# Kernel optimization log

Measured on AMD Instinct MI355X. Metric: run time of the kernel, lower is better.

Reference implementation:

```python
import jax, jax.numpy as jnp
import numpy as np

N = 4096        # nodes
F_IN = 256      # in_features
F_OUT = 64      # out_features
H = 64          # lstm_out_features
MAX_DEG = 64    # max neighbor count == max packed seq length
ALPHA = 0.2     # leaky relu negative slope
NEG = -9e15


def setup_inputs() -> dict:
    key = jax.random.key(0)
    ks = jax.random.split(key, 8)
    h = jax.random.normal(ks[0], (N, F_IN), dtype=jnp.float32)
    # per-node neighbor counts in [1, MAX_DEG]
    seq_length = jax.random.randint(ks[1], (N,), 1, MAX_DEG + 1, dtype=jnp.int32)
    # adjacency with exactly seq_length[i] ones in row i
    r = jax.random.uniform(ks[2], (N, N))
    ranks = jnp.argsort(jnp.argsort(-r, axis=1), axis=1)
    adj = (ranks < seq_length[:, None]).astype(jnp.float32)
    # parameters (xavier-ish scale)
    W = jax.random.normal(ks[3], (F_IN, F_OUT), dtype=jnp.float32) * (2.0 / (F_IN + F_OUT)) ** 0.5
    a = jax.random.normal(ks[4], (2 * F_OUT, 1), dtype=jnp.float32) * 0.1
    # backward-direction LSTM weights (torch gate order i,f,g,o); forward dir is unused in output
    w_ih = jax.random.normal(ks[5], (4 * H, F_OUT), dtype=jnp.float32) * 0.1
    w_hh = jax.random.normal(ks[6], (4 * H, H), dtype=jnp.float32) * 0.1
    b_ih = jnp.zeros((4 * H,), dtype=jnp.float32)
    b_hh = jnp.zeros((4 * H,), dtype=jnp.float32)
    return {"h": h, "adj": adj, "seq_length": seq_length, "W": W, "a": a,
            "w_ih": w_ih, "w_hh": w_hh, "b_ih": b_ih, "b_hh": b_hh}


def reference(h, adj, seq_length, W, a, w_ih, w_hh, b_ih, b_hh):
    n = h.shape[0]
    Wh = h @ W                                   # [N, F_OUT]
    # e[i,j] = leakyrelu(a_left . Wh_i + a_right . Wh_j)  (same math as O(N^2) concat)
    a1, a2 = a[:F_OUT, 0], a[F_OUT:, 0]
    e = jax.nn.leaky_relu((Wh @ a1)[:, None] + (Wh @ a2)[None, :], negative_slope=ALPHA)
    att = jax.nn.softmax(jnp.where(adj > 0, e, NEG), axis=1)   # [N, N]
    Wh2 = att @ Wh                               # aggregated node features [N, F_OUT]
    # sort neighbors by descending attention; LSTM only reads the first seq_length[i] <= MAX_DEG
    order = jnp.argsort(-att, axis=1)[:, :MAX_DEG]            # [N, T]
    seq = Wh2[order]                              # [N, T, F_OUT]
    # backward LSTM direction == run forward over the length-reversed sequence
    t = jnp.arange(MAX_DEG)
    rev_idx = jnp.clip(seq_length[:, None] - 1 - t[None, :], 0)
    rev = jnp.take_along_axis(seq, rev_idx[:, :, None], axis=1)  # [N, T, F_OUT]
    mask = t[None, :] < seq_length[:, None]                       # [N, T]

    def cell(carry, xm):
        hs, cs = carry
        x, m = xm                                 # x: [N, F_OUT], m: [N]
        gates = x @ w_ih.T + hs @ w_hh.T + b_ih + b_hh
        i, f, g, o = jnp.split(gates, 4, axis=1)
        c_new = jax.nn.sigmoid(f) * cs + jax.nn.sigmoid(i) * jnp.tanh(g)
        h_new = jax.nn.sigmoid(o) * jnp.tanh(c_new)
        m = m[:, None]
        return (jnp.where(m, h_new, hs), jnp.where(m, c_new, cs)), None

    init = (jnp.zeros((n, H), Wh.dtype), jnp.zeros((n, H), Wh.dtype))
    xs = (jnp.swapaxes(rev, 0, 1), mask.T)        # time-major
    (hn, _), _ = jax.lax.scan(cell, init, xs)
    return hn                                     # [N, H]  == torch hn[-1] (backward dir)
```

## Files before the change

kernel.cpp:

```cpp
#include <hip/hip_runtime.h>
#include <hip/hip_bf16.h>
#include <math.h>

#define N_NODES 4096
#define F_INN   256
#define F_OUTT  64
#define HID     64
#define MAXDEG  64

typedef __attribute__((ext_vector_type(8))) short bf16x8;
typedef __attribute__((ext_vector_type(4))) float f32x4;

__device__ int    g_mode;
__device__ int    g_anyArr[64];
__device__ float  g_Wh [N_NODES * F_OUTT];
__device__ float  g_s1 [N_NODES];
__device__ float  g_s2 [N_NODES];
__device__ int    g_rev[N_NODES * MAXDEG];
__device__ int    g_perm[N_NODES];
__device__ int    g_nbr[N_NODES * MAXDEG];
__device__ int    g_cnt[N_NODES];
__device__ float4 g_GX [N_NODES * F_OUTT];

__device__ __forceinline__ float bf2f(unsigned short u) {
  union { unsigned int i; float f; } v; v.i = ((unsigned int)u) << 16; return v.f;
}
__device__ __forceinline__ unsigned short f2bf(float f) {
  union { __hip_bfloat16 b; unsigned short u; } v; v.b = __float2bfloat16(f); return v.u;
}

__device__ __forceinline__ float bcastf(float v, int l) {
  return __int_as_float(__builtin_amdgcn_readlane(__float_as_int(v), l));
}

__device__ __forceinline__ float rcp_fast(float x) { return __builtin_amdgcn_rcpf(x); }

__device__ __forceinline__ float sigm(float x) {
  return rcp_fast(1.f + __expf(-x));
}
__device__ __forceinline__ float tanh_fast(float x) {
  return fmaf(-2.f, rcp_fast(1.f + __expf(2.f * x)), 1.f);
}

__device__ __forceinline__ int mbcnt64(unsigned long long m) {
  return __builtin_amdgcn_mbcnt_hi((unsigned)(m >> 32),
         __builtin_amdgcn_mbcnt_lo((unsigned)(m & 0xFFFFFFFFull), 0));
}

__device__ __forceinline__ bf16x8 zfrag() {
  bf16x8 z;
  #pragma unroll
  for (int i = 0; i < 8; i++) z[i] = 0;
  return z;
}

__device__ __forceinline__ void block_sync_lds() {
  __asm__ volatile("s_waitcnt lgkmcnt(0)" ::: "memory");
  __builtin_amdgcn_s_barrier();
}

#define MFMA16(a, b, c) __builtin_amdgcn_mfma_f32_16x16x32_bf16((a), (b), (c), 0, 0, 0)

__global__ __launch_bounds__(256) void k_detect(const unsigned int* __restrict__ aw) {
  __shared__ int any;
  if (threadIdx.x == 0) any = 0;
  __syncthreads();
  const uint4 v = ((const uint4*)aw)[blockIdx.x * 256 + threadIdx.x];
  int loc = (int)((v.x & 0xFFFFu) | (v.y & 0xFFFFu) | (v.z & 0xFFFFu) | (v.w & 0xFFFFu));
  if (loc) atomicOr(&any, 1);
  __syncthreads();
  if (threadIdx.x == 0) g_anyArr[blockIdx.x] = any;
}

__global__ __launch_bounds__(256) void k_sort(const int* __restrict__ seq) {
  __shared__ int hist[MAXDEG + 1];
  __shared__ int offs[MAXDEG + 1];
  const int tid = threadIdx.x;
  if (tid <= MAXDEG) hist[tid] = 0;
  __syncthreads();
  if (tid == 0) {
    int any = 0;
    for (int b = 0; b < 64; b++) any |= g_anyArr[b];
    g_mode = any ? 1 : 0;
  }
  for (int i = tid; i < N_NODES; i += 256)
    atomicAdd(&hist[min(max(seq[i], 0), MAXDEG)], 1);
  __syncthreads();
  if (tid == 0) {
    int run = 0;
    for (int L = MAXDEG; L >= 0; L--) { offs[L] = run; run += hist[L]; }
  }
  __syncthreads();
  for (int i = tid; i < N_NODES; i += 256) {
    int p = atomicAdd(&offs[min(max(seq[i], 0), MAXDEG)], 1);
    g_perm[p] = i;
  }
}

__global__ __launch_bounds__(256) void k_scan(const void* __restrict__ adj) {
  const bool bf16 = (g_mode == 1);
  const int i = blockIdx.x;
  const int w = threadIdx.x >> 6, lane = threadIdx.x & 63;
  __shared__ int seg[4][MAXDEG];
  __shared__ int scnt[4];

  int base = 0;
  if (bf16) {
    const uint4* ar = (const uint4*)((const unsigned short*)adj + (size_t)i * N_NODES);
    #pragma unroll
    for (int it = 0; it < 2; it++) {
      const uint4 v = ar[w * 128 + it * 64 + lane];
      unsigned word[4] = {v.x, v.y, v.z, v.w};
      bool nz[8];
      #pragma unroll
      for (int k = 0; k < 4; k++) {
        nz[2 * k]     = (word[k] & 0x0000FFFFu) != 0u;
        nz[2 * k + 1] = (word[k] & 0xFFFF0000u) != 0u;
      }
      int pre = 0, tot = 0;
      #pragma unroll
      for (int k = 0; k < 8; k++) {
        unsigned long long bl = __ballot(nz[k]);
        pre += mbcnt64(bl);
        tot += __popcll(bl);
      }
      int loc = 0;
      #pragma unroll
      for (int k = 0; k < 8; k++) {
        if (nz[k]) {
          int p = base + pre + loc;
          if (p < MAXDEG) seg[w][p] = w * 1024 + it * 512 + lane * 8 + k;
          loc++;
        }
      }
      base += tot;
    }
  } else {
    const float4* ar = (const float4*)((const float*)adj + (size_t)i * N_NODES);
    #pragma unroll
    for (int it = 0; it < 4; it++) {
      const float4 v = ar[w * 256 + it * 64 + lane];
      bool nz[4] = {v.x != 0.0f, v.y != 0.0f, v.z != 0.0f, v.w != 0.0f};
      int pre = 0, tot = 0;
      #pragma unroll
      for (int k = 0; k < 4; k++) {
        unsigned long long bl = __ballot(nz[k]);
        pre += mbcnt64(bl);
        tot += __popcll(bl);
      }
      int loc = 0;
      #pragma unroll
      for (int k = 0; k < 4; k++) {
        if (nz[k]) {
          int p = base + pre + loc;
          if (p < MAXDEG) seg[w][p] = w * 1024 + it * 256 + lane * 4 + k;
          loc++;
        }
      }
      base += tot;
    }
  }
  if (lane == 0) scnt[w] = base;
  __syncthreads();
  int off = 0;
  #pragma unroll
  for (int u = 0; u < 4; u++) off += (u < w) ? scnt[u] : 0;
  const int cw = min(scnt[w], MAXDEG);
  if (lane < cw) {
    const int p = off + lane;
    if (p < MAXDEG) g_nbr[i * MAXDEG + p] = seg[w][lane];
  }
  if (threadIdx.x == 0)
    g_cnt[i] = min(scnt[0] + scnt[1] + scnt[2] + scnt[3], MAXDEG);
}

__global__ __launch_bounds__(256) void k_wh(
    const void* __restrict__ h, const void* __restrict__ W, const void* __restrict__ a)
{
  const bool bf16 = (g_mode == 1);
  __shared__ float Ws[F_INN * F_OUTT];
  const int tid = threadIdx.x;
  if (bf16) {
    const ushort4* Wu = (const ushort4*)W;
    for (int v = tid; v < F_INN * F_OUTT / 4; v += 256) {
      ushort4 u = Wu[v];
      ((float4*)Ws)[v] = make_float4(bf2f(u.x), bf2f(u.y), bf2f(u.z), bf2f(u.w));
    }
  } else {
    const float4* Wf = (const float4*)W;
    for (int v = tid; v < F_INN * F_OUTT / 4; v += 256) ((float4*)Ws)[v] = Wf[v];
  }
  __syncthreads();
  const int wave = tid >> 6, lane = tid & 63;
  const int row = blockIdx.x * 4 + wave;
  float hr0, hr1, hr2, hr3;
  if (bf16) {
    ushort4 v = ((const ushort4*)((const unsigned short*)h + row * F_INN))[lane];
    hr0 = bf2f(v.x); hr1 = bf2f(v.y); hr2 = bf2f(v.z); hr3 = bf2f(v.w);
  } else {
    float4 v = ((const float4*)((const float*)h + row * F_INN))[lane];
    hr0 = v.x; hr1 = v.y; hr2 = v.z; hr3 = v.w;
  }
  double acc = 0.0;
  #pragma unroll 8
  for (int l = 0; l < 64; l++) {
    float h0 = bcastf(hr0, l), h1 = bcastf(hr1, l);
    float h2 = bcastf(hr2, l), h3 = bcastf(hr3, l);
    acc += (double)h0 * (double)Ws[(l * 4 + 0) * F_OUTT + lane];
    acc += (double)h1 * (double)Ws[(l * 4 + 1) * F_OUTT + lane];
    acc += (double)h2 * (double)Ws[(l * 4 + 2) * F_OUTT + lane];
    acc += (double)h3 * (double)Ws[(l * 4 + 3) * F_OUTT + lane];
  }
  const float whv = (float)acc;
  g_Wh[row * F_OUTT + lane] = whv;
  float a1, a2;
  if (bf16) {
    a1 = bf2f(((const unsigned short*)a)[lane]);
    a2 = bf2f(((const unsigned short*)a)[F_OUTT + lane]);
  } else {
    a1 = ((const float*)a)[lane];
    a2 = ((const float*)a)[F_OUTT + lane];
  }
  double t1 = (double)whv * (double)a1;
  double t2 = (double)whv * (double)a2;
  #pragma unroll
  for (int off = 32; off > 0; off >>= 1) {
    t1 += __shfl_down(t1, off);
    t2 += __shfl_down(t2, off);
  }
  if (lane == 0) { g_s1[row] = (float)t1; g_s2[row] = (float)t2; }
}

__global__ __launch_bounds__(256) void k_att2(
    const void* __restrict__ w_ih,
    const void* __restrict__ b_ih, const void* __restrict__ b_hh)
{
  const bool bf16 = (g_mode == 1);
  const int wv = threadIdx.x >> 6, lane = threadIdx.x & 63;
  const int i = blockIdx.x * 4 + wv;

  __shared__ int   s_nbr[4][MAXDEG];
  __shared__ float s_att[4][MAXDEG];
  __shared__ int   s_srt[4][MAXDEG];
  __shared__ float s_wh2[4][F_OUTT];
  int*   nbr  = s_nbr[wv];
  float* attp = s_att[wv];
  int*   srt  = s_srt[wv];
  float* wh2  = s_wh2[wv];

  const int L = min(g_cnt[i], MAXDEG);
  int jn = 0;
  if (lane < L) jn = g_nbr[i * MAXDEG + lane] & (N_NODES - 1);
  nbr[lane] = jn;

  const float s2v = g_s2[jn];
  float av;
  {
    float s = g_s1[i] + s2v;
    float e = (s > 0.0f) ? s : 0.2f * s;
    if (lane >= L) e = -3.0e38f;
    float m = e;
    #pragma unroll
    for (int off = 32; off > 0; off >>= 1) m = fmaxf(m, __shfl_xor(m, off));
    float p = (lane < L) ? __expf(e - m) : 0.0f;
    float ssum = p;
    #pragma unroll
    for (int off = 32; off > 0; off >>= 1) ssum += __shfl_xor(ssum, off);
    av = p * rcp_fast(ssum);
    attp[lane] = av;
    int rank = 0;
    for (int qq = 0; qq < L; qq++) {
      float aq = __shfl(av, qq);
      int   jq = __shfl(jn, qq);
      rank += (aq > av || (aq == av && jq < jn)) ? 1 : 0;
    }
    if (lane < L) srt[rank] = jn;
  }
  g_rev[i * MAXDEG + lane] = (lane < L) ? srt[L - 1 - lane] : 0;

  float a0 = 0.f, a1 = 0.f, a2 = 0.f, a3 = 0.f;
  int q = 0;
  for (; q + 4 <= L; q += 4) {
    const int j0 = nbr[q], j1 = nbr[q + 1], j2 = nbr[q + 2], j3 = nbr[q + 3];
    const float t0 = attp[q], t1 = attp[q + 1], t2 = attp[q + 2], t3 = attp[q + 3];
    a0 = fmaf(t0, g_Wh[(size_t)j0 * F_OUTT + lane], a0);
    a1 = fmaf(t1, g_Wh[(size_t)j1 * F_OUTT + lane], a1);
    a2 = fmaf(t2, g_Wh[(size_t)j2 * F_OUTT + lane], a2);
    a3 = fmaf(t3, g_Wh[(size_t)j3 * F_OUTT + lane], a3);
  }
  for (; q < L; q++) {
    const int j0 = nbr[q];
    a0 = fmaf(attp[q], g_Wh[(size_t)j0 * F_OUTT + lane], a0);
  }
  wh2[lane] = (a0 + a1) + (a2 + a3);

  float gx[4] = {0.f, 0.f, 0.f, 0.f};
  if (bf16) {
    #pragma unroll
    for (int g = 0; g < 4; g++) {
      const unsigned short* wr = (const unsigned short*)w_ih + (size_t)(g * 64 + lane) * F_OUTT;
      #pragma unroll
      for (int ch = 0; ch < 8; ch++) {
        bf16x8 vv = *(const bf16x8*)(wr + ch * 8);
        #pragma unroll
        for (int e2 = 0; e2 < 8; e2++)
          gx[g] = fmaf(bf2f((unsigned short)vv[e2]), wh2[ch * 8 + e2], gx[g]);
      }
      gx[g] += bf2f(((const unsigned short*)b_ih)[g * 64 + lane]) +
               bf2f(((const unsigned short*)b_hh)[g * 64 + lane]);
    }
  } else {
    #pragma unroll
    for (int g = 0; g < 4; g++) {
      const float* wr = (const float*)w_ih + (size_t)(g * 64 + lane) * F_OUTT;
      #pragma unroll
      for (int ch = 0; ch < 16; ch++) {
        float4 vv = *(const float4*)(wr + ch * 4);
        gx[g] = fmaf(vv.x, wh2[ch * 4 + 0], gx[g]);
        gx[g] = fmaf(vv.y, wh2[ch * 4 + 1], gx[g]);
        gx[g] = fmaf(vv.z, wh2[ch * 4 + 2], gx[g]);
        gx[g] = fmaf(vv.w, wh2[ch * 4 + 3], gx[g]);
      }
      gx[g] += ((const float*)b_ih)[g * 64 + lane] + ((const float*)b_hh)[g * 64 + lane];
    }
  }
  g_GX[(size_t)i * F_OUTT + lane] = make_float4(gx[0], gx[1], gx[2], gx[3]);
}

__global__ __launch_bounds__(256, 1) void k_lstm_mfma(
    const void* __restrict__ w_hh, const int* __restrict__ seq,
    void* __restrict__ out)
{
  const bool bf16 = (g_mode == 1);
  __shared__ __align__(16) unsigned short lds_h[2][16 * 72];
  __shared__ int lds_idx[16][MAXDEG];
  const int tid = threadIdx.x;
  const int w = tid >> 6, lane = tid & 63;
  const int q = lane >> 4, c = lane & 15;
  const int rb = blockIdx.x * 16;

  for (int v = tid; v < 16 * MAXDEG; v += 256) {
    const int e = v >> 6, t0 = v & (MAXDEG - 1);
    const int row = g_perm[rb + e] & (N_NODES - 1);
    lds_idx[e][t0] = g_rev[row * MAXDEG + t0] & (N_NODES - 1);
  }

  const int Lmax = min(max(seq[g_perm[rb] & (N_NODES - 1)], 0), MAXDEG);
  int row_e[4], Ls_e[4];
  #pragma unroll
  for (int r = 0; r < 4; r++) {
    row_e[r] = g_perm[rb + q * 4 + r] & (N_NODES - 1);
    Ls_e[r]  = min(max(seq[row_e[r]], 0), MAXDEG);
  }
  const int d_unit = 16 * w + c;

  bf16x8 Bhi[4][2];
  #pragma unroll
  for (int g = 0; g < 4; g++) {
    const int col = 64 * g + d_unit;
    #pragma unroll
    for (int ch = 0; ch < 2; ch++) {
      if (bf16) {
        Bhi[g][ch] = *(const bf16x8*)((const unsigned short*)w_hh + (size_t)col * 64 + ch * 32 + q * 8);
      } else {
        const float* wp = (const float*)w_hh + (size_t)col * 64 + ch * 32 + q * 8;
        float4 va = *(const float4*)wp, vb = *(const float4*)(wp + 4);
        bf16x8 f;
        f[0] = (short)f2bf(va.x); f[1] = (short)f2bf(va.y);
        f[2] = (short)f2bf(va.z); f[3] = (short)f2bf(va.w);
        f[4] = (short)f2bf(vb.x); f[5] = (short)f2bf(vb.y);
        f[6] = (short)f2bf(vb.z); f[7] = (short)f2bf(vb.w);
        Bhi[g][ch] = f;
      }
    }
  }

  __syncthreads();

  float4 gxb[4][4];
  #pragma unroll
  for (int s = 0; s < 4; s++) {
    #pragma unroll
    for (int r = 0; r < 4; r++)
      gxb[s][r] = g_GX[lds_idx[q * 4 + r][s] * F_OUTT + d_unit];
  }
  int idx_cur[4];
  #pragma unroll
  for (int r = 0; r < 4; r++) idx_cur[r] = lds_idx[q * 4 + r][4];

  bf16x8 h0 = zfrag(), h1 = zfrag();
  float cst[4] = {0.f, 0.f, 0.f, 0.f}, hst[4] = {0.f, 0.f, 0.f, 0.f};
  const int Lr = (Lmax + 3) & ~3;

  for (int t = 0; t < Lr; t += 4) {
    #pragma unroll
    for (int j = 0; j < 4; j++) {
      const int tt = t + j;
      f32x4 acc[4];
      #pragma unroll
      for (int g = 0; g < 4; g++) {
        f32x4 a;
        a[0] = (g==0)?gxb[j][0].x:(g==1)?gxb[j][0].y:(g==2)?gxb[j][0].z:gxb[j][0].w;
        a[1] = (g==0)?gxb[j][1].x:(g==1)?gxb[j][1].y:(g==2)?gxb[j][1].z:gxb[j][1].w;
        a[2] = (g==0)?gxb[j][2].x:(g==1)?gxb[j][2].y:(g==2)?gxb[j][2].z:gxb[j][2].w;
        a[3] = (g==0)?gxb[j][3].x:(g==1)?gxb[j][3].y:(g==2)?gxb[j][3].z:gxb[j][3].w;
        a = MFMA16(h0, Bhi[g][0], a);
        a = MFMA16(h1, Bhi[g][1], a);
        acc[g] = a;
      }
      #pragma unroll
      for (int r = 0; r < 4; r++)
        gxb[j][r] = g_GX[idx_cur[r] * F_OUTT + d_unit];
      {
        const int nt = min(tt + 5, MAXDEG - 1);
        #pragma unroll
        for (int r = 0; r < 4; r++) idx_cur[r] = lds_idx[q * 4 + r][nt];
      }
      unsigned short* lh = lds_h[j & 1];
      #pragma unroll
      for (int r = 0; r < 4; r++) {
        float ig = sigm(acc[0][r]);
        float fg = sigm(acc[1][r]);
        float gg = tanh_fast(acc[2][r]);
        float og = sigm(acc[3][r]);
        float cn = fg * cst[r] + ig * gg;
        float hn = og * tanh_fast(cn);
        bool live = (tt < Ls_e[r]);
        cst[r] = live ? cn : cst[r];
        hst[r] = live ? hn : hst[r];
        lh[(q * 4 + r) * 72 + d_unit] = f2bf(hst[r]);
      }
      block_sync_lds();
      {
        const unsigned short* lr_ = lds_h[j & 1] + c * 72;
        h0 = *(const bf16x8*)(lr_ + 8 * q);
        h1 = *(const bf16x8*)(lr_ + 32 + 8 * q);
      }
    }
  }
  #pragma unroll
  for (int r = 0; r < 4; r++) {
    if (bf16) ((__hip_bfloat16*)out)[row_e[r] * HID + d_unit] = __float2bfloat16(hst[r]);
    else      ((float*)out)[row_e[r] * HID + d_unit] = hst[r];
  }
}

extern "C" void kernel_launch(void* const* d_in, const int* in_sizes, int n_in,
                              void* d_out, int out_size, void* d_ws, size_t ws_size,
                              hipStream_t stream) {
  (void)in_sizes; (void)n_in; (void)out_size; (void)d_ws; (void)ws_size;
  const void* h    = d_in[0];
  const void* adj  = d_in[1];
  const int*  seq  = (const int*)d_in[2];
  const void* W    = d_in[3];
  const void* a    = d_in[4];
  const void* w_ih = d_in[5];
  const void* w_hh = d_in[6];
  const void* b_ih = d_in[7];
  const void* b_hh = d_in[8];

  k_detect   <<<64,           256, 0, stream>>>((const unsigned int*)adj);
  k_sort     <<<1,            256, 0, stream>>>(seq);
  k_scan     <<<N_NODES,      256, 0, stream>>>(adj);
  k_wh       <<<N_NODES / 4,  256, 0, stream>>>(h, W, a);
  k_att2     <<<N_NODES / 4,  256, 0, stream>>>(w_ih, b_ih, b_hh);
  k_lstm_mfma<<<N_NODES / 16, 256, 0, stream>>>(w_hh, seq, d_out);
}
```

Baseline: 227.4 us.

## Halve LSTM rows per block and redistribute gate math via lane shuffles

The LSTM kernel now handles 8 nodes per block instead of 16, which doubles the grid to 512 blocks, and it raises launch bounds to allow 2 blocks per CU. The MFMA still computes 16 rows, with rows 8-15 clamped to duplicates. Gate results are shuffled across lanes so each lane evaluates only 2 rows of sigmoid/tanh instead of 4. This aims to fill more CUs and cut the per-step elementwise latency on the serial recurrence, at the cost of half-wasted MFMA work, extra shuffles, and more total gather traffic.

```diff
diff --git a/kernel.cpp b/kernel.cpp
--- a/kernel.cpp
+++ b/kernel.cpp
@@ -327,32 +327,41 @@
   g_GX[(size_t)i * F_OUTT + lane] = make_float4(gx[0], gx[1], gx[2], gx[3]);
 }
 
-__global__ __launch_bounds__(256, 1) void k_lstm_mfma(
+__global__ __launch_bounds__(256, 2) void k_lstm_mfma(
     const void* __restrict__ w_hh, const int* __restrict__ seq,
     void* __restrict__ out)
 {
   const bool bf16 = (g_mode == 1);
   __shared__ __align__(16) unsigned short lds_h[2][16 * 72];
-  __shared__ int lds_idx[16][MAXDEG];
+  __shared__ int lds_idx[8][MAXDEG];
   const int tid = threadIdx.x;
   const int w = tid >> 6, lane = tid & 63;
   const int q = lane >> 4, c = lane & 15;
-  const int rb = blockIdx.x * 16;
-
-  for (int v = tid; v < 16 * MAXDEG; v += 256) {
+  const int rb = blockIdx.x * 8;
+
+  for (int v = tid; v < 2 * 16 * 72; v += 256) ((unsigned short*)lds_h)[v] = 0;
+
+  for (int v = tid; v < 8 * MAXDEG; v += 256) {
     const int e = v >> 6, t0 = v & (MAXDEG - 1);
     const int row = g_perm[rb + e] & (N_NODES - 1);
     lds_idx[e][t0] = g_rev[row * MAXDEG + t0] & (N_NODES - 1);
   }
 
   const int Lmax = min(max(seq[g_perm[rb] & (N_NODES - 1)], 0), MAXDEG);
-  int row_e[4], Ls_e[4];
-  #pragma unroll
-  for (int r = 0; r < 4; r++) {
-    row_e[r] = g_perm[rb + q * 4 + r] & (N_NODES - 1);
-    Ls_e[r]  = min(max(seq[row_e[r]], 0), MAXDEG);
+
+  int rows_c[4];
+  #pragma unroll
+  for (int r = 0; r < 4; r++) rows_c[r] = min(q * 4 + r, 7);
+
+  int row_own[2], Ls_own[2];
+  #pragma unroll
+  for (int k = 0; k < 2; k++) {
+    row_own[k] = g_perm[rb + 2 * q + k] & (N_NODES - 1);
+    Ls_own[k]  = min(max(seq[row_own[k]], 0), MAXDEG);
   }
   const int d_unit = 16 * w + c;
+  const int sl = ((lane >> 5) << 4) | c;
+  const bool qodd = (q & 1) != 0;
 
   bf16x8 Bhi[4][2];
   #pragma unroll
@@ -382,14 +391,14 @@
   for (int s = 0; s < 4; s++) {
     #pragma unroll
     for (int r = 0; r < 4; r++)
-      gxb[s][r] = g_GX[lds_idx[q * 4 + r][s] * F_OUTT + d_unit];
+      gxb[s][r] = g_GX[lds_idx[rows_c[r]][s] * F_OUTT + d_unit];
   }
   int idx_cur[4];
   #pragma unroll
-  for (int r = 0; r < 4; r++) idx_cur[r] = lds_idx[q * 4 + r][4];
+  for (int r = 0; r < 4; r++) idx_cur[r] = lds_idx[rows_c[r]][4];
 
   bf16x8 h0 = zfrag(), h1 = zfrag();
-  float cst[4] = {0.f, 0.f, 0.f, 0.f}, hst[4] = {0.f, 0.f, 0.f, 0.f};
+  float cst[2] = {0.f, 0.f}, hst[2] = {0.f, 0.f};
   const int Lr = (Lmax + 3) & ~3;
 
   for (int t = 0; t < Lr; t += 4) {
@@ -414,21 +423,31 @@
       {
         const int nt = min(tt + 5, MAXDEG - 1);
         #pragma unroll
-        for (int r = 0; r < 4; r++) idx_cur[r] = lds_idx[q * 4 + r][nt];
+        for (int r = 0; r < 4; r++) idx_cur[r] = lds_idx[rows_c[r]][nt];
+      }
+      float gv[4][2];
+      #pragma unroll
+      for (int g = 0; g < 4; g++) {
+        float t0v = __shfl(acc[g][0], sl);
+        float t1v = __shfl(acc[g][1], sl);
+        float t2v = __shfl(acc[g][2], sl);
+        float t3v = __shfl(acc[g][3], sl);
+        gv[g][0] = qodd ? t2v : t0v;
+        gv[g][1] = qodd ? t3v : t1v;
       }
       unsigned short* lh = lds_h[j & 1];
       #pragma unroll
-      for (int r = 0; r < 4; r++) {
-        float ig = sigm(acc[0][r]);
-        float fg = sigm(acc[1][r]);
-        float gg = tanh_fast(acc[2][r]);
-        float og = sigm(acc[3][r]);
-        float cn = fg * cst[r] + ig * gg;
+      for (int k = 0; k < 2; k++) {
+        float ig = sigm(gv[0][k]);
+        float fg = sigm(gv[1][k]);
+        float gg = tanh_fast(gv[2][k]);
+        float og = sigm(gv[3][k]);
+        float cn = fg * cst[k] + ig * gg;
         float hn = og * tanh_fast(cn);
-        bool live = (tt < Ls_e[r]);
-        cst[r] = live ? cn : cst[r];
-        hst[r] = live ? hn : hst[r];
-        lh[(q * 4 + r) * 72 + d_unit] = f2bf(hst[r]);
+        bool live = (tt < Ls_own[k]);
+        cst[k] = live ? cn : cst[k];
+        hst[k] = live ? hn : hst[k];
+        lh[(2 * q + k) * 72 + d_unit] = f2bf(hst[k]);
       }
       block_sync_lds();
       {
@@ -439,9 +458,9 @@
     }
   }
   #pragma unroll
-  for (int r = 0; r < 4; r++) {
-    if (bf16) ((__hip_bfloat16*)out)[row_e[r] * HID + d_unit] = __float2bfloat16(hst[r]);
-    else      ((float*)out)[row_e[r] * HID + d_unit] = hst[r];
+  for (int k = 0; k < 2; k++) {
+    if (bf16) ((__hip_bfloat16*)out)[row_own[k] * HID + d_unit] = __float2bfloat16(hst[k]);
+    else      ((float*)out)[row_own[k] * HID + d_unit] = hst[k];
   }
 }
 
@@ -464,5 +483,5 @@
   k_scan     <<<N_NODES,      256, 0, stream>>>(adj);
   k_wh       <<<N_NODES / 4,  256, 0, stream>>>(h, W, a);
   k_att2     <<<N_NODES / 4,  256, 0, stream>>>(w_ih, b_ih, b_hh);
-  k_lstm_mfma<<<N_NODES / 16, 256, 0, stream>>>(w_hh, seq, d_out);
-}
+  k_lstm_mfma<<<N_NODES / 8,  256, 0, stream>>>(w_hh, seq, d_out);
+}
```

After: 231.5 us. No clear change (+1.8%).
